# Kernel tuning notes

Hardware: AMD Instinct MI355X
Metric: run time of the kernel (lower is better)

The kernel has to match this reference:

```python
import jax, jax.numpy as jnp
import numpy as np

NUM_EMBEDDINGS = 512
EMBEDDING_DIM = 64
COMMITMENT_COST = 0.25


def setup_inputs() -> dict:
    key = jax.random.key(0)
    k1, k2 = jax.random.split(key)
    inputs = jax.random.normal(k1, (32, EMBEDDING_DIM, 64, 64), dtype=jnp.float32)
    # nn.Embedding weight init: uniform(-1/K, 1/K)
    weight = jax.random.uniform(
        k2, (NUM_EMBEDDINGS, EMBEDDING_DIM), dtype=jnp.float32,
        minval=-1.0 / NUM_EMBEDDINGS, maxval=1.0 / NUM_EMBEDDINGS)
    return {"inputs": inputs, "weight": weight}


def reference(inputs, weight):
    # NCHW -> NHWC
    x = jnp.transpose(inputs, (0, 2, 3, 1))
    B, H, W, D = x.shape
    flat = x.reshape(-1, D)  # [N, D]
    # squared L2 distances to each code: [N, K]
    distances = (jnp.sum(flat * flat, axis=1, keepdims=True)
                 - 2.0 * flat @ weight.T
                 + jnp.sum(weight * weight, axis=1))
    idx = jnp.argmin(distances, axis=1)  # [N]
    # one-hot @ weight == gather (one-hot entries are exactly 0/1)
    quantized = jnp.take(weight, idx, axis=0).reshape(B, H, W, D)
    e_latent_loss = jnp.mean((jax.lax.stop_gradient(quantized) - x) ** 2)
    q_latent_loss = jnp.mean((quantized - jax.lax.stop_gradient(x)) ** 2)
    loss = q_latent_loss + COMMITMENT_COST * e_latent_loss
    # straight-through estimator
    quantized_st = x + jax.lax.stop_gradient(quantized - x)
    discrete_latent = idx.reshape(B, H, W)
    quantized_out = jnp.transpose(quantized_st, (0, 3, 1, 2))  # NHWC -> NCHW
    return discrete_latent, quantized_out, loss
```

## Files before the change

kernel.cpp:

```cpp
#include <hip/hip_runtime.h>

typedef unsigned long long ull;

#define NUM_K   512
#define DIM     64
#define N_ROWS  (32 * 64 * 64)
#define HW      4096
#define CHW     (64 * 4096)

#define IDX_OFF  0
#define Q_OFF    N_ROWS
#define LOSS_OFF (N_ROWS + 32 * 64 * 4096)

#define CAP     8
#define TILE_R  128
#define NBLK    (N_ROWS / TILE_R)

#define WK1S    1.0e-4f
#define WK2S    2.0e-5f

#define WS_W2_OFF    32768
#define WS_W2H_OFF   33280
#define WS_SWMAX_OFF 33792
#define WS_LSL_BYTE  147456
#define WS_NEED      (147456 + NBLK * 8)

typedef __attribute__((ext_vector_type(8)))  short bf16x8;
typedef __attribute__((ext_vector_type(16))) float f32x16;

typedef unsigned uGLB __attribute__((address_space(1)));
typedef unsigned uLDS __attribute__((address_space(3)));
#define GLD16(g, l) __builtin_amdgcn_global_load_lds((const uGLB*)(g), (uLDS*)(l), 16, 0, 0)

#define NP_SUMSQ64(SRC, DST)                                                   \
    do {                                                                       \
        float r_[8];                                                           \
        _Pragma("unroll")                                                      \
        for (int j_ = 0; j_ < 8; ++j_) r_[j_] = __fmul_rn((SRC)[j_], (SRC)[j_]); \
        _Pragma("unroll")                                                      \
        for (int i_ = 8; i_ < 64; i_ += 8) {                                   \
            _Pragma("unroll")                                                  \
            for (int j_ = 0; j_ < 8; ++j_)                                     \
                r_[j_] = __fadd_rn(r_[j_], __fmul_rn((SRC)[i_ + j_], (SRC)[i_ + j_])); \
        }                                                                      \
        (DST) = __fadd_rn(__fadd_rn(__fadd_rn(r_[0], r_[1]), __fadd_rn(r_[2], r_[3])), \
                          __fadd_rn(__fadd_rn(r_[4], r_[5]), __fadd_rn(r_[6], r_[7]))); \
    } while (0)

#define NP_SUMSQ64_G(XC, DST)                                                  \
    do {                                                                       \
        float r_[8];                                                           \
        _Pragma("unroll")                                                      \
        for (int j_ = 0; j_ < 8; ++j_) {                                       \
            float v_ = (XC)[(size_t)j_ * HW];                                  \
            r_[j_] = __fmul_rn(v_, v_);                                        \
        }                                                                      \
        _Pragma("unroll")                                                      \
        for (int i_ = 8; i_ < 64; i_ += 8) {                                   \
            _Pragma("unroll")                                                  \
            for (int j_ = 0; j_ < 8; ++j_) {                                   \
                float v_ = (XC)[(size_t)(i_ + j_) * HW];                       \
                r_[j_] = __fadd_rn(r_[j_], __fmul_rn(v_, v_));                 \
            }                                                                  \
        }                                                                      \
        (DST) = __fadd_rn(__fadd_rn(__fadd_rn(r_[0], r_[1]), __fadd_rn(r_[2], r_[3])), \
                          __fadd_rn(__fadd_rn(r_[4], r_[5]), __fadd_rn(r_[6], r_[7]))); \
    } while (0)

__device__ __forceinline__ unsigned bf16rn(float f) {
    unsigned u = __float_as_uint(f);
    return (u + 0x7fffu + ((u >> 16) & 1u)) >> 16;
}
__device__ __forceinline__ float bf2f(unsigned h) { return __uint_as_float(h << 16); }

__device__ __forceinline__ float evald(const float* __restrict__ xr,
                                       const float* __restrict__ wc,
                                       float A, float w2c) {
    float m = 0.0f;
    #pragma unroll
    for (int d = 0; d < DIM; ++d) m = __fmaf_rn(xr[d], wc[d], m);
    return __fadd_rn(__fsub_rn(A, __fmul_rn(2.0f, m)), w2c);
}
__device__ __forceinline__ float evald_g(const float* __restrict__ xcol,
                                         const float* __restrict__ wc,
                                         float A, float w2c) {
    float m = 0.0f;
    #pragma unroll
    for (int d = 0; d < DIM; ++d) m = __fmaf_rn(xcol[(size_t)d * HW], wc[d], m);
    return __fadd_rn(__fsub_rn(A, __fmul_rn(2.0f, m)), w2c);
}

__global__ __launch_bounds__(64) void vq_prep8(const float* __restrict__ weight,
                                               unsigned* __restrict__ ws) {
    const int c = blockIdx.x * 64 + threadIdx.x;
    const int T = c >> 5, m = c & 31;
    const float* wr = weight + c * DIM;
    float wv[DIM];
    #pragma unroll
    for (int d = 0; d < DIM; d += 4) {
        float4 t4 = *(const float4*)&wr[d];
        wv[d] = t4.x; wv[d + 1] = t4.y; wv[d + 2] = t4.z; wv[d + 3] = t4.w;
    }
    float s; NP_SUMSQ64(wv, s);
    ((float*)(ws + WS_W2_OFF))[c]  = s;
    ((float*)(ws + WS_W2H_OFF))[c] = 0.5f * s;
    float sa = 0.0f;
    #pragma unroll
    for (int d = 0; d < DIM; ++d) sa = __fadd_rn(sa, fabsf(wv[d]));
    float sv = sa * 1.0002f + 1e-7f;

    #pragma unroll
    for (int s4 = 0; s4 < 4; ++s4) {
        const int gH = T * 8 + s4 * 2, gL = gH + 1;
        #pragma unroll
        for (int kh = 0; kh < 2; ++kh) {
            unsigned hu[4], lu[4];
            #pragma unroll
            for (int p = 0; p < 4; ++p) {
                float e0 = wv[16 * s4 + 8 * kh + 2 * p];
                float e1 = wv[16 * s4 + 8 * kh + 2 * p + 1];
                unsigned h0 = bf16rn(e0), h1 = bf16rn(e1);
                float r0 = __fsub_rn(e0, bf2f(h0));
                float r1 = __fsub_rn(e1, bf2f(h1));
                hu[p] = h0 | (h1 << 16);
                lu[p] = bf16rn(r0) | (bf16rn(r1) << 16);
            }
            const int slot = (m + 32 * kh) * 4;
            *(uint4*)&ws[gH * 256 + slot] = make_uint4(hu[0], hu[1], hu[2], hu[3]);
            *(uint4*)&ws[gL * 256 + slot] = make_uint4(lu[0], lu[1], lu[2], lu[3]);
        }
    }
    #pragma unroll
    for (int mk = 1; mk <= 32; mk <<= 1) sv = fmaxf(sv, __shfl_xor(sv, mk));
    if (threadIdx.x == 0) ((float*)(ws + WS_SWMAX_OFF))[blockIdx.x] = sv;
}

__global__ __launch_bounds__(256, 3) void vq_mfma10(const float* __restrict__ x_in,
                                                    const float* __restrict__ weight,
                                                    const unsigned* __restrict__ frg,
                                                    double* __restrict__ lslots,
                                                    float* __restrict__ out) {
    __shared__ __align__(16) unsigned dbuf[2][4096];
    __shared__ __align__(16) float w2h_l[NUM_K];
    __shared__ __align__(16) float w2a_l[NUM_K];
    __shared__ int   cntL[TILE_R];
    __shared__ unsigned short listL[TILE_R * CAP];
    __shared__ int   ilds[TILE_R];
    __shared__ float wsum[4];

    const int tid   = threadIdx.x;
    const int lane  = tid & 63;
    const int wid   = tid >> 6;
    const int wbase = wid * 32;
    const int n31   = lane & 31;
    const int kh    = lane >> 5;

    const int rowbase = blockIdx.x * TILE_R;
    const int b       = rowbase >> 12;
    const int hw0     = rowbase & 4095;
    const float* xb   = x_in + (size_t)b * CHW + hw0;

    #pragma unroll
    for (int i = 0; i < 4; ++i) {
        int sg = wid * 4 + i;
        GLD16(frg + sg * 256 + lane * 4, &dbuf[0][sg * 256]);
    }
    if (wid == 0)      GLD16(frg + WS_W2H_OFF       + lane * 4, (unsigned*)&w2h_l[0]);
    else if (wid == 1) GLD16(frg + WS_W2H_OFF + 256 + lane * 4, (unsigned*)&w2h_l[256]);
    else if (wid == 2) GLD16(frg + WS_W2_OFF        + lane * 4, (unsigned*)&w2a_l[0]);
    else               GLD16(frg + WS_W2_OFF  + 256 + lane * 4, (unsigned*)&w2a_l[256]);

    bf16x8 bh[4], bl[4];
    float xreg[32];
    float mx = 0.0f;
    const float* xp = xb + wbase + n31;
    #pragma unroll
    for (int s = 0; s < 4; ++s) {
        union { unsigned u[4]; bf16x8 v; } ch, cl;
        #pragma unroll
        for (int p = 0; p < 4; ++p) {
            const int k0 = 16 * s + 8 * kh + 2 * p;
            float x0 = xp[(size_t)k0 * HW];
            float x1 = xp[(size_t)(k0 + 1) * HW];
            xreg[8 * s + 2 * p]     = x0;
            xreg[8 * s + 2 * p + 1] = x1;
            mx = fmaxf(mx, fmaxf(fabsf(x0), fabsf(x1)));
            float e0 = -x0, e1 = -x1;
            unsigned h0 = bf16rn(e0), h1 = bf16rn(e1);
            float r0 = __fsub_rn(e0, bf2f(h0));
            float r1 = __fsub_rn(e1, bf2f(h1));
            ch.u[p] = h0 | (h1 << 16);
            cl.u[p] = bf16rn(r0) | (bf16rn(r1) << 16);
        }
        bh[s] = ch.v;
        bl[s] = cl.v;
    }
    mx = fmaxf(mx, __shfl_xor(mx, 32));
    if (tid < TILE_R) cntL[tid] = 0;

    const float* swp = (const float*)(frg + WS_SWMAX_OFF);
    float SWMAX = swp[0];
    #pragma unroll
    for (int i = 1; i < 8; ++i) SWMAX = fmaxf(SWMAX, swp[i]);
    const float gthr = __fmaf_rn(WK1S * mx, 2.0f * SWMAX, WK2S);
    float thr = 3.4e38f;
    __syncthreads();

    for (int c = 0; c < 8; ++c) {
        const int par = c & 1;
        if (c < 7) {
            const int nxt = par ^ 1;
            #pragma unroll
            for (int i = 0; i < 4; ++i) {
                int sg = wid * 4 + i;
                GLD16(frg + (c + 1) * 4096 + sg * 256 + lane * 4,
                      &dbuf[nxt][sg * 256]);
            }
        }

        f32x16 acc0, acc1;
        {
            const float* wa = &w2h_l[(2 * c) * 32 + 4 * kh];
            float4 a0 = *(const float4*)&wa[0];
            float4 a1 = *(const float4*)&wa[8];
            float4 a2 = *(const float4*)&wa[16];
            float4 a3 = *(const float4*)&wa[24];
            acc0[0]=a0.x; acc0[1]=a0.y; acc0[2]=a0.z; acc0[3]=a0.w;
            acc0[4]=a1.x; acc0[5]=a1.y; acc0[6]=a1.z; acc0[7]=a1.w;
            acc0[8]=a2.x; acc0[9]=a2.y; acc0[10]=a2.z; acc0[11]=a2.w;
            acc0[12]=a3.x; acc0[13]=a3.y; acc0[14]=a3.z; acc0[15]=a3.w;
            const float* wb = &w2h_l[(2 * c + 1) * 32 + 4 * kh];
            float4 c0 = *(const float4*)&wb[0];
            float4 c1 = *(const float4*)&wb[8];
            float4 c2 = *(const float4*)&wb[16];
            float4 c3 = *(const float4*)&wb[24];
            acc1[0]=c0.x; acc1[1]=c0.y; acc1[2]=c0.z; acc1[3]=c0.w;
            acc1[4]=c1.x; acc1[5]=c1.y; acc1[6]=c1.z; acc1[7]=c1.w;
            acc1[8]=c2.x; acc1[9]=c2.y; acc1[10]=c2.z; acc1[11]=c2.w;
            acc1[12]=c3.x; acc1[13]=c3.y; acc1[14]=c3.z; acc1[15]=c3.w;
        }

        #pragma unroll
        for (int s = 0; s < 4; ++s) {
            bf16x8 ah0 = *(const bf16x8*)&dbuf[par][(s * 2 + 0) * 256 + lane * 4];
            bf16x8 al0 = *(const bf16x8*)&dbuf[par][(s * 2 + 1) * 256 + lane * 4];
            bf16x8 ah1 = *(const bf16x8*)&dbuf[par][(8 + s * 2 + 0) * 256 + lane * 4];
            bf16x8 al1 = *(const bf16x8*)&dbuf[par][(8 + s * 2 + 1) * 256 + lane * 4];
            acc0 = __builtin_amdgcn_mfma_f32_32x32x16_bf16(ah0, bh[s], acc0, 0, 0, 0);
            acc1 = __builtin_amdgcn_mfma_f32_32x32x16_bf16(ah1, bh[s], acc1, 0, 0, 0);
            acc0 = __builtin_amdgcn_mfma_f32_32x32x16_bf16(al0, bh[s], acc0, 0, 0, 0);
            acc1 = __builtin_amdgcn_mfma_f32_32x32x16_bf16(al1, bh[s], acc1, 0, 0, 0);
            acc0 = __builtin_amdgcn_mfma_f32_32x32x16_bf16(ah0, bl[s], acc0, 0, 0, 0);
            acc1 = __builtin_amdgcn_mfma_f32_32x32x16_bf16(ah1, bl[s], acc1, 0, 0, 0);
        }

        #pragma unroll
        for (int tl = 0; tl < 2; ++tl) {
            float tmin = 3.4e38f;
            #pragma unroll
            for (int r = 0; r < 16; ++r)
                tmin = fminf(tmin, (tl ? acc1[r] : acc0[r]));
            float tlr = fminf(tmin, __shfl_xor(tmin, 32));
            thr = fminf(thr, __fadd_rn(tlr, gthr));
            if (tmin <= thr) {
                const int cb = (2 * c + tl) * 32 + 4 * kh;
                const int rr = wbase + n31;
                #pragma unroll
                for (int r = 0; r < 16; ++r) {
                    float tv = (tl ? acc1[r] : acc0[r]);
                    if (tv <= thr) {
                        int code = cb + (r & 3) + 8 * (r >> 2);
                        int cn = atomicAdd(&cntL[rr], 1);
                        if (cn < CAP) listL[rr * CAP + cn] = (unsigned short)code;
                    }
                }
            }
        }

        __syncthreads();
    }

    if (lane < 32) {
        const int r   = wbase + lane;
        const int cnt = cntL[r];
        if (cnt == 1) {
            int bi = listL[r * CAP];
            ilds[r] = bi;
            out[IDX_OFF + rowbase + r] = (float)bi;
        } else if (cnt >= 2 && cnt <= CAP) {
            const float* xcol = xb + r;
            float A; NP_SUMSQ64_G(xcol, A);
            float bd = 3.4e38f; int bi = 1 << 30;
            for (int t2 = 0; t2 < cnt; ++t2) {
                int cd = listL[r * CAP + t2];
                float d2 = evald_g(xcol, weight + cd * DIM, A, w2a_l[cd]);
                if (d2 < bd || (d2 == bd && cd < bi)) { bd = d2; bi = cd; }
            }
            ilds[r] = bi;
            out[IDX_OFF + rowbase + r] = (float)bi;
        }
    }
    for (int rr = 0; rr < 32; ++rr) {
        int r   = wbase + rr;
        int cnt = cntL[r];
        if (cnt < 1 || cnt > CAP) {
            const float* xcol = xb + r;
            float A; NP_SUMSQ64_G(xcol, A);
            float bd = 3.4e38f; int bi = 1 << 30;
            #pragma unroll
            for (int t2 = 0; t2 < 8; ++t2) {
                int cd = t2 * 64 + lane;
                float d2 = evald_g(xcol, weight + cd * DIM, A, w2a_l[cd]);
                if (d2 < bd || (d2 == bd && cd < bi)) { bd = d2; bi = cd; }
            }
            ull key = ((ull)__float_as_uint(bd) << 32) | (unsigned)bi;
            #pragma unroll
            for (int mk = 1; mk <= 32; mk <<= 1) {
                ull o = __shfl_xor(key, mk);
                if (o < key) key = o;
            }
            if (lane == 0) {
                int bi2 = (int)(key & 0xffffffffu);
                ilds[r] = bi2;
                out[IDX_OFF + rowbase + r] = (float)bi2;
            }
        }
    }
    __syncthreads();

    {
        const int row = wbase + n31;
        const int bi  = ilds[row];
        const float* wrow = weight + bi * DIM;
        float* ob = out + Q_OFF + (size_t)b * CHW + hw0 + row;
        float lsum = 0.0f;
        #pragma unroll
        for (int s = 0; s < 4; ++s) {
            #pragma unroll
            for (int e = 0; e < 8; ++e) {
                const int k = 16 * s + 8 * kh + e;
                float xd   = xreg[8 * s + e];
                float wq   = wrow[k];
                float diff = __fsub_rn(wq, xd);
                ob[(size_t)k * HW] = __fadd_rn(xd, diff);
                lsum = fmaf(diff, diff, lsum);
            }
        }
        #pragma unroll
        for (int off = 32; off > 0; off >>= 1) lsum += __shfl_down(lsum, off);
        if (lane == 0) wsum[wid] = lsum;
    }
    __syncthreads();
    if (tid == 0) {
        double s = 0.0;
        #pragma unroll
        for (int i = 0; i < 4; ++i) s += (double)wsum[i];
        lslots[blockIdx.x] = s;
    }
}

__global__ void vq_finalizeN(const double* __restrict__ lslots, int n,
                             float* __restrict__ out) {
    double s = 0.0;
    for (int i = threadIdx.x; i < n; i += 64) s += lslots[i];
    #pragma unroll
    for (int off = 32; off > 0; off >>= 1) s += __shfl_down(s, off);
    if (threadIdx.x == 0) {
        double m = s / 8388608.0;
        out[LOSS_OFF] = (float)(m + 0.25 * m);
    }
}

__global__ void vq_zero(double* __restrict__ loss_acc) {
    if (threadIdx.x == 0) *loss_acc = 0.0;
}

__global__ __launch_bounds__(256) void vq_fused(const float* __restrict__ x_in,
                                                const float* __restrict__ weight,
                                                double* __restrict__ loss_acc,
                                                float* __restrict__ out) {
    __shared__ float w2s[NUM_K];
    for (int k = threadIdx.x; k < NUM_K; k += 256) {
        const float* wk = weight + k * DIM;
        float s; NP_SUMSQ64(wk, s);
        w2s[k] = s;
    }
    __syncthreads();

    const int n  = blockIdx.x * 256 + threadIdx.x;
    const int b  = n >> 12;
    const int hw = n & 4095;
    const float* xp = x_in + b * CHW + hw;
    float x[DIM];
    #pragma unroll
    for (int d = 0; d < DIM; ++d) x[d] = xp[d * HW];

    float A; NP_SUMSQ64(x, A);

    float best = 3.4e38f;
    int   bi   = 0;
    for (int k = 0; k < NUM_K; k += 4) {
        const float* w0 = weight + k * DIM;
        float m0 = 0.f, m1 = 0.f, m2 = 0.f, m3 = 0.f;
        #pragma unroll
        for (int d = 0; d < DIM; ++d) {
            float xd = x[d];
            m0 = __fmaf_rn(xd, w0[d],           m0);
            m1 = __fmaf_rn(xd, w0[DIM + d],     m1);
            m2 = __fmaf_rn(xd, w0[2 * DIM + d], m2);
            m3 = __fmaf_rn(xd, w0[3 * DIM + d], m3);
        }
        float d0 = __fadd_rn(__fsub_rn(A, __fmul_rn(2.0f, m0)), w2s[k]);
        float d1 = __fadd_rn(__fsub_rn(A, __fmul_rn(2.0f, m1)), w2s[k + 1]);
        float d2 = __fadd_rn(__fsub_rn(A, __fmul_rn(2.0f, m2)), w2s[k + 2]);
        float d3 = __fadd_rn(__fsub_rn(A, __fmul_rn(2.0f, m3)), w2s[k + 3]);
        if (d0 < best) { best = d0; bi = k; }
        if (d1 < best) { best = d1; bi = k + 1; }
        if (d2 < best) { best = d2; bi = k + 2; }
        if (d3 < best) { best = d3; bi = k + 3; }
    }
    const int idx = bi;

    out[IDX_OFF + n] = (float)idx;
    const float* qrow = weight + idx * DIM;
    float* oq = out + Q_OFF + b * CHW + hw;
    float lsum = 0.0f;
    #pragma unroll
    for (int d = 0; d < DIM; ++d) {
        float xd   = xp[d * HW];
        float diff = __fsub_rn(qrow[d], xd);
        oq[d * HW] = __fadd_rn(xd, diff);
        lsum = fmaf(diff, diff, lsum);
    }
    #pragma unroll
    for (int off = 32; off > 0; off >>= 1) lsum += __shfl_down(lsum, off);
    __shared__ float wsum[4];
    if ((threadIdx.x & 63) == 0) wsum[threadIdx.x >> 6] = lsum;
    __syncthreads();
    if (threadIdx.x == 0)
        atomicAdd(loss_acc, (double)((wsum[0] + wsum[1]) + (wsum[2] + wsum[3])));
}

__global__ void vq_finalize(const double* __restrict__ loss_acc,
                            float* __restrict__ out) {
    double m = *loss_acc / 8388608.0;
    out[LOSS_OFF] = (float)(m + 0.25 * m);
}

extern "C" void kernel_launch(void* const* d_in, const int* in_sizes, int n_in,
                              void* d_out, int out_size, void* d_ws, size_t ws_size,
                              hipStream_t stream) {
    const float* x = (const float*)d_in[0];
    const float* w = (const float*)d_in[1];
    float* out = (float*)d_out;

    if (ws_size >= WS_NEED) {
        unsigned* ws32 = (unsigned*)d_ws;
        double* lslots = (double*)((char*)d_ws + WS_LSL_BYTE);
        vq_prep8<<<8, 64, 0, stream>>>(w, ws32);
        vq_mfma10<<<NBLK, 256, 0, stream>>>(x, w, ws32, lslots, out);
        vq_finalizeN<<<1, 64, 0, stream>>>(lslots, NBLK, out);
    } else {
        double* loss_acc = (double*)d_ws;
        vq_zero<<<1, 64, 0, stream>>>(loss_acc);
        vq_fused<<<512, 256, 0, stream>>>(x, w, loss_acc, out);
        vq_finalize<<<1, 1, 0, stream>>>(loss_acc, out);
    }
}
```

Measured before the change: 179.1 us.

## Drop xreg register cache and fuse loss finalize via last-block atomic counter

The main VQ kernel no longer keeps 32 input values per thread in registers across the distance phase. It re-reads x from global memory in the epilogue instead, with each half-wave handling 32 contiguous dims. This lowers register pressure and may help occupancy, at the cost of a second read of x that will likely hit cache. The separate finalize kernel is also removed: blocks atomically add their partial loss to one double, and the last block to bump a counter writes the final loss. This saves a launch but makes the summation order nondeterministic.

```diff
diff --git a/kernel.cpp b/kernel.cpp
--- a/kernel.cpp
+++ b/kernel.cpp
@@ -23,7 +23,7 @@
 #define WS_W2H_OFF   33280
 #define WS_SWMAX_OFF 33792
 #define WS_LSL_BYTE  147456
-#define WS_NEED      (147456 + NBLK * 8)
+#define WS_NEED      (147456 + 16)
 
 typedef __attribute__((ext_vector_type(8)))  short bf16x8;
 typedef __attribute__((ext_vector_type(16))) float f32x16;
@@ -92,6 +92,10 @@
 
 __global__ __launch_bounds__(64) void vq_prep8(const float* __restrict__ weight,
                                                unsigned* __restrict__ ws) {
+    if (blockIdx.x == 0 && threadIdx.x == 0) {
+        *(double*)((char*)ws + WS_LSL_BYTE) = 0.0;
+        *(unsigned*)((char*)ws + WS_LSL_BYTE + 8) = 0u;
+    }
     const int c = blockIdx.x * 64 + threadIdx.x;
     const int T = c >> 5, m = c & 31;
     const float* wr = weight + c * DIM;
@@ -135,10 +139,10 @@
     if (threadIdx.x == 0) ((float*)(ws + WS_SWMAX_OFF))[blockIdx.x] = sv;
 }
 
-__global__ __launch_bounds__(256, 3) void vq_mfma10(const float* __restrict__ x_in,
+__global__ __launch_bounds__(256, 3) void vq_mfma11(const float* __restrict__ x_in,
                                                     const float* __restrict__ weight,
                                                     const unsigned* __restrict__ frg,
-                                                    double* __restrict__ lslots,
+                                                    double* __restrict__ lossacc,
                                                     float* __restrict__ out) {
     __shared__ __align__(16) unsigned dbuf[2][4096];
     __shared__ __align__(16) float w2h_l[NUM_K];
@@ -171,7 +175,6 @@
     else               GLD16(frg + WS_W2_OFF  + 256 + lane * 4, (unsigned*)&w2a_l[256]);
 
     bf16x8 bh[4], bl[4];
-    float xreg[32];
     float mx = 0.0f;
     const float* xp = xb + wbase + n31;
     #pragma unroll
@@ -182,8 +185,6 @@
             const int k0 = 16 * s + 8 * kh + 2 * p;
             float x0 = xp[(size_t)k0 * HW];
             float x1 = xp[(size_t)(k0 + 1) * HW];
-            xreg[8 * s + 2 * p]     = x0;
-            xreg[8 * s + 2 * p + 1] = x1;
             mx = fmaxf(mx, fmaxf(fabsf(x0), fabsf(x1)));
             float e0 = -x0, e1 = -x1;
             unsigned h0 = bf16rn(e0), h1 = bf16rn(e1);
@@ -328,46 +329,38 @@
     }
     __syncthreads();
 
-    {
-        const int row = wbase + n31;
-        const int bi  = ilds[row];
-        const float* wrow = weight + bi * DIM;
-        float* ob = out + Q_OFF + (size_t)b * CHW + hw0 + row;
-        float lsum = 0.0f;
-        #pragma unroll
-        for (int s = 0; s < 4; ++s) {
-            #pragma unroll
-            for (int e = 0; e < 8; ++e) {
-                const int k = 16 * s + 8 * kh + e;
-                float xd   = xreg[8 * s + e];
-                float wq   = wrow[k];
-                float diff = __fsub_rn(wq, xd);
-                ob[(size_t)k * HW] = __fadd_rn(xd, diff);
-                lsum = fmaf(diff, diff, lsum);
-            }
-        }
-        #pragma unroll
-        for (int off = 32; off > 0; off >>= 1) lsum += __shfl_down(lsum, off);
-        if (lane == 0) wsum[wid] = lsum;
-    }
+    const int row = wbase + (lane & 31);
+    const int dh  = (lane >> 5) << 5;
+    const float* xcol = xb + row;
+    const float* wr2  = weight + ilds[row] * DIM + dh;
+    float* ob = out + Q_OFF + (size_t)b * CHW + hw0 + row;
+    float lsum = 0.0f;
+    #pragma unroll
+    for (int j = 0; j < 32; ++j) {
+        float xd   = xcol[(size_t)(dh + j) * HW];
+        float wq   = wr2[j];
+        float diff = __fsub_rn(wq, xd);
+        ob[(size_t)(dh + j) * HW] = __fadd_rn(xd, diff);
+        lsum = fmaf(diff, diff, lsum);
+    }
+    #pragma unroll
+    for (int off = 32; off > 0; off >>= 1) lsum += __shfl_down(lsum, off);
+    if (lane == 0) wsum[wid] = lsum;
     __syncthreads();
+
     if (tid == 0) {
         double s = 0.0;
         #pragma unroll
         for (int i = 0; i < 4; ++i) s += (double)wsum[i];
-        lslots[blockIdx.x] = s;
-    }
-}
-
-__global__ void vq_finalizeN(const double* __restrict__ lslots, int n,
-                             float* __restrict__ out) {
-    double s = 0.0;
-    for (int i = threadIdx.x; i < n; i += 64) s += lslots[i];
-    #pragma unroll
-    for (int off = 32; off > 0; off >>= 1) s += __shfl_down(s, off);
-    if (threadIdx.x == 0) {
-        double m = s / 8388608.0;
-        out[LOSS_OFF] = (float)(m + 0.25 * m);
+        unsigned* acnt = (unsigned*)(lossacc + 1);
+        atomicAdd(lossacc, s);
+        asm volatile("s_waitcnt vmcnt(0)" ::: "memory");
+        unsigned prev = atomicAdd(acnt, 1u);
+        if (prev == (unsigned)(NBLK - 1)) {
+            double tot = atomicAdd(lossacc, 0.0);
+            double m = tot / 8388608.0;
+            out[LOSS_OFF] = (float)(m + 0.25 * m);
+        }
     }
 }
 
@@ -456,10 +449,9 @@
 
     if (ws_size >= WS_NEED) {
         unsigned* ws32 = (unsigned*)d_ws;
-        double* lslots = (double*)((char*)d_ws + WS_LSL_BYTE);
+        double* lossacc = (double*)((char*)d_ws + WS_LSL_BYTE);
         vq_prep8<<<8, 64, 0, stream>>>(w, ws32);
-        vq_mfma10<<<NBLK, 256, 0, stream>>>(x, w, ws32, lslots, out);
-        vq_finalizeN<<<1, 64, 0, stream>>>(lslots, NBLK, out);
+        vq_mfma11<<<NBLK, 256, 0, stream>>>(x, w, ws32, lossacc, out);
     } else {
         double* loss_acc = (double*)d_ws;
         vq_zero<<<1, 64, 0, stream>>>(loss_acc);
```

New measurement: 167.0 us. 6.8% less time.
